# Kernel optimization log

Measured on AMD Instinct MI355X. Metric: run time of the kernel, lower is better.

The kernel has to match this reference:

```python
import jax, jax.numpy as jnp
import numpy as np
import math

NUM_EMBED = 1024
EMBED_FEATS = 256
IN_FEATS = 512
COMMITMENT_COST = 0.25
B, T = 16, 4096


def setup_inputs() -> dict:
    key = jax.random.key(0)
    k1, k2, k3, k4 = jax.random.split(key, 4)
    inputs = jax.random.normal(k1, (B, IN_FEATS, T), dtype=jnp.float32)
    # Conv1d(kernel_size=1) == per-position linear: weight [E, C_in], bias [E]
    proj_w = jax.random.normal(k2, (EMBED_FEATS, IN_FEATS), dtype=jnp.float32) / np.sqrt(IN_FEATS)
    proj_b = jax.random.normal(k3, (EMBED_FEATS,), dtype=jnp.float32) * 0.01
    embed = jax.random.normal(k4, (NUM_EMBED, EMBED_FEATS), dtype=jnp.float32)
    return {"inputs": inputs, "proj_w": proj_w, "proj_b": proj_b, "embed": embed}


def reference(inputs, proj_w, proj_b, embed):
    sg = jax.lax.stop_gradient
    b, c_in, t = inputs.shape
    # 1x1 conv projection then transpose(1,-1): [B, T, E]
    x = jnp.einsum('bct,ec->bte', inputs, proj_w) + proj_b
    flat = x.reshape(-1, EMBED_FEATS)  # [B*T, E]
    d2 = (jnp.sum(flat * flat, axis=1, keepdims=True)
          + jnp.sum(embed * embed, axis=1)
          - 2.0 * flat @ embed.T)  # [B*T, num_embed]
    q_idx = jnp.argmin(d2, axis=1)  # [B*T]
    # one-hot @ embed == direct gather (same math, same gradient structure)
    z_q = embed[q_idx].reshape(x.shape)  # [B, T, E]
    vq_loss = jnp.mean((z_q - sg(x)) ** 2)
    commitment_loss = jnp.mean((sg(z_q) - x) ** 2)
    loss = vq_loss + COMMITMENT_COST * commitment_loss
    z_q_st = x + sg(z_q - x)  # straight-through
    n_tokens = flat.shape[0]
    probs = jnp.zeros((NUM_EMBED,), dtype=jnp.float32).at[q_idx].add(1.0) / n_tokens
    log_perplexity = -jnp.sum(probs * jnp.log(probs + 1e-10))
    num_spatial = n_tokens / b
    kldiv_r = math.log(NUM_EMBED) * num_spatial * jnp.ones((b, 1), dtype=jnp.float32)
    z_q_out = jnp.swapaxes(z_q_st, 1, 2)  # [B, E, T]
    return z_q_out, loss, kldiv_r, log_perplexity
```

## Files before the change

kernel.cpp:

```cpp
#include <hip/hip_runtime.h>
#include <hip/hip_bf16.h>
#include <math.h>

#define TT   4096
#define BB   16
#define NTOK 65536
#define CIN  512
#define EF   256
#define NE   1024

typedef __attribute__((ext_vector_type(8))) short bf16x8;
typedef __attribute__((ext_vector_type(4))) float f32x4;

static __device__ __forceinline__ unsigned short f2bf(float f) {
  unsigned int u = __float_as_uint(f);
  u += 0x7fffu + ((u >> 16) & 1u);
  return (unsigned short)(u >> 16);
}

#define GLL(gsrc, ldst) \
  __builtin_amdgcn_global_load_lds((const __attribute__((address_space(1))) void*)(gsrc), \
                                   (__attribute__((address_space(3))) void*)(ldst), 16, 0, 0)

__global__ __launch_bounds__(256) void k_prep(const float* __restrict__ Wf,
                                              const float* __restrict__ Ef,
                                              unsigned short* __restrict__ Wbf,
                                              unsigned short* __restrict__ Ebf,
                                              float* __restrict__ e_norm) {
  int bid = blockIdx.x;
  if (bid < 512) {
    int i = bid * 256 + threadIdx.x;
    Wbf[i] = f2bf(Wf[i]);
  } else if (bid < 1536) {
    int i = (bid - 512) * 256 + threadIdx.x;
    Ebf[i] = f2bf(-2.0f * Ef[i]);
  } else {
    int w = threadIdx.x >> 6, l = threadIdx.x & 63;
    int k = (bid - 1536) * 4 + w;
    const float4 v4 = ((const float4*)(Ef + (size_t)k * EF))[l];
    float s = v4.x * v4.x + v4.y * v4.y + v4.z * v4.z + v4.w * v4.w;
    for (int off = 32; off; off >>= 1) s += __shfl_down(s, off);
    if (l == 0) e_norm[k] = s;
  }
}

__global__ __launch_bounds__(256, 2) void k_fused(const float* __restrict__ in,
                                                  const unsigned short* __restrict__ Wbf,
                                                  const float* __restrict__ bias,
                                                  const unsigned short* __restrict__ Ebf,
                                                  const float* __restrict__ e_norm,
                                                  int* __restrict__ bi_out,
                                                  unsigned int* __restrict__ hist,
                                                  float* __restrict__ sse) {
  __shared__ unsigned short lds[24576];
  unsigned short* as_ = lds;
  unsigned short* bs = lds + 4096;
  unsigned short* xs = lds;
  unsigned short* es = lds + 16384;

  int tid = threadIdx.x;
  int w = tid >> 6, l = tid & 63;
  int l15 = l & 15, quad = l >> 4;
  int tok0 = blockIdx.x * 64;
  int bidx = tok0 >> 12;
  int tg0 = tok0 & 4095;
  const float* src = in + (size_t)bidx * CIN * TT + tg0;

  f32x4 acc[4][4];
#pragma unroll
  for (int a = 0; a < 4; ++a)
#pragma unroll
    for (int b = 0; b < 4; ++b) acc[a][b] = (f32x4){0.f, 0.f, 0.f, 0.f};

  for (int ks = 0; ks < 8; ++ks) {
    int k0 = ks * 64;
#pragma unroll
    for (int i = 0; i < 8; ++i) {
      int g = i * 256 + tid;
      int row = g >> 3, pc = g & 7, lc = pc ^ (row & 7);
      GLL(Wbf + (size_t)row * CIN + k0 + lc * 8, bs + g * 8);
    }
#pragma unroll
    for (int cc = 0; cc < 2; ++cc) {
      float v[8];
      const float* s0 = src + (size_t)(k0 + w * 16 + cc * 8) * TT + l;
#pragma unroll
      for (int i = 0; i < 8; ++i) v[i] = s0[(size_t)i * TT];
      alignas(16) unsigned short tmp[8];
#pragma unroll
      for (int j = 0; j < 8; ++j) tmp[j] = f2bf(v[j]);
      int c8 = w * 2 + cc;
      int pc = c8 ^ (l & 7);
      *(bf16x8*)(as_ + l * 64 + pc * 8) = *(const bf16x8*)tmp;
    }
    __syncthreads();
#pragma unroll
    for (int s = 0; s < 2; ++s) {
      int lcb = s * 4 + quad;
      bf16x8 af[4], bfr[4];
#pragma unroll
      for (int msub = 0; msub < 4; ++msub) {
        int row = msub * 16 + l15;
        int pc = lcb ^ (row & 7);
        af[msub] = *(const bf16x8*)(as_ + row * 64 + pc * 8);
      }
#pragma unroll
      for (int nsub = 0; nsub < 4; ++nsub) {
        int row = w * 64 + nsub * 16 + l15;
        int pc = lcb ^ (row & 7);
        bfr[nsub] = *(const bf16x8*)(bs + row * 64 + pc * 8);
      }
#pragma unroll
      for (int msub = 0; msub < 4; ++msub)
#pragma unroll
        for (int nsub = 0; nsub < 4; ++nsub)
          acc[msub][nsub] = __builtin_amdgcn_mfma_f32_16x16x32_bf16(af[msub], bfr[nsub],
                                                                    acc[msub][nsub], 0, 0, 0);
    }
    __syncthreads();
  }

  float xsq = 0.f;
#pragma unroll
  for (int nsub = 0; nsub < 4; ++nsub) {
    float bv = bias[w * 64 + nsub * 16 + l15];
    int e = w * 64 + nsub * 16 + l15;
    int cx = e >> 3;
#pragma unroll
    for (int msub = 0; msub < 4; ++msub)
#pragma unroll
      for (int reg = 0; reg < 4; ++reg) {
        int m = msub * 16 + quad * 4 + reg;
        float x = acc[msub][nsub][reg] + bv;
        xsq += x * x;
        int pcx = cx ^ (m & 31);
        xs[m * 256 + pcx * 8 + (e & 7)] = f2bf(x);
      }
  }
  __syncthreads();

  float best_v[4][4];
  int best_i[4][4];
#pragma unroll
  for (int a = 0; a < 4; ++a)
#pragma unroll
    for (int b = 0; b < 4; ++b) { best_v[a][b] = 3.0e38f; best_i[a][b] = 0; }

  for (int chunk = 0; chunk < 8; ++chunk) {
    int c0 = chunk * 128;
    f32x4 dacc[4][2];
#pragma unroll
    for (int nsub = 0; nsub < 2; ++nsub) {
      float en = e_norm[c0 + w * 32 + nsub * 16 + l15];
#pragma unroll
      for (int msub = 0; msub < 4; ++msub) dacc[msub][nsub] = (f32x4){en, en, en, en};
    }
    for (int ks = 0; ks < 4; ++ks) {
      int k0 = ks * 64;
#pragma unroll
      for (int i = 0; i < 4; ++i) {
        int g = i * 256 + tid;
        int row = g >> 3, pc = g & 7, lc = pc ^ (row & 7);
        GLL(Ebf + (size_t)(c0 + row) * EF + k0 + lc * 8, es + g * 8);
      }
      __syncthreads();
#pragma unroll
      for (int s = 0; s < 2; ++s) {
        bf16x8 af[4], bfr[2];
        int cx = ks * 8 + s * 4 + quad;
#pragma unroll
        for (int msub = 0; msub < 4; ++msub) {
          int row = msub * 16 + l15;
          int pcx = cx ^ (row & 31);
          af[msub] = *(const bf16x8*)(xs + row * 256 + pcx * 8);
        }
        int ck = s * 4 + quad;
#pragma unroll
        for (int nsub = 0; nsub < 2; ++nsub) {
          int row = w * 32 + nsub * 16 + l15;
          int pc = ck ^ (row & 7);
          bfr[nsub] = *(const bf16x8*)(es + row * 64 + pc * 8);
        }
#pragma unroll
        for (int msub = 0; msub < 4; ++msub)
#pragma unroll
          for (int nsub = 0; nsub < 2; ++nsub)
            dacc[msub][nsub] = __builtin_amdgcn_mfma_f32_16x16x32_bf16(af[msub], bfr[nsub],
                                                                       dacc[msub][nsub], 0, 0, 0);
      }
      __syncthreads();
    }
#pragma unroll
    for (int msub = 0; msub < 4; ++msub)
#pragma unroll
      for (int nsub = 0; nsub < 2; ++nsub) {
        int code = c0 + w * 32 + nsub * 16 + l15;
#pragma unroll
        for (int reg = 0; reg < 4; ++reg) {
          float v = dacc[msub][nsub][reg];
          if (v < best_v[msub][reg]) { best_v[msub][reg] = v; best_i[msub][reg] = code; }
        }
      }
  }

#pragma unroll
  for (int msub = 0; msub < 4; ++msub)
#pragma unroll
    for (int reg = 0; reg < 4; ++reg) {
      float v = best_v[msub][reg];
      int idx = best_i[msub][reg];
#pragma unroll
      for (int off = 8; off; off >>= 1) {
        float ov = __shfl_xor(v, off, 16);
        int oi = __shfl_xor(idx, off, 16);
        if (ov < v || (ov == v && oi < idx)) { v = ov; idx = oi; }
      }
      best_v[msub][reg] = v;
      best_i[msub][reg] = idx;
    }
  float* red_v = (float*)es;
  int* red_i = (int*)(es) + 256;
  float* xred = (float*)(es) + 512;
  if (l15 == 0) {
#pragma unroll
    for (int msub = 0; msub < 4; ++msub)
#pragma unroll
      for (int reg = 0; reg < 4; ++reg) {
        int m = msub * 16 + quad * 4 + reg;
        red_v[w * 64 + m] = best_v[msub][reg];
        red_i[w * 64 + m] = best_i[msub][reg];
      }
  }
  for (int off = 32; off; off >>= 1) xsq += __shfl_down(xsq, off);
  if (l == 0) xred[w] = xsq;
  __syncthreads();
  if (tid < 64) {
    float v = red_v[tid];
    int idx = red_i[tid];
#pragma unroll
    for (int wj = 1; wj < 4; ++wj) {
      float ov = red_v[wj * 64 + tid];
      int oi = red_i[wj * 64 + tid];
      if (ov < v || (ov == v && oi < idx)) { v = ov; idx = oi; }
    }
    bi_out[tok0 + tid] = idx;
    atomicAdd(&hist[idx], 1u);
    float sv = v;
    for (int off = 32; off; off >>= 1) sv += __shfl_down(sv, off);
    if (tid == 0) atomicAdd(sse, sv + xred[0] + xred[1] + xred[2] + xred[3]);
  }
}

__global__ __launch_bounds__(256) void k_gather(const float* __restrict__ embed,
                                                const int* __restrict__ bi,
                                                float* __restrict__ out) {
  __shared__ float zq[128 * 65];
  __shared__ int idxs[128];
  int tid = threadIdx.x;
  int tok0 = blockIdx.x * 128;
  int e0 = blockIdx.y * 64;
  if (tid < 128) idxs[tid] = bi[tok0 + tid];
  __syncthreads();
  int l15 = tid & 15, tg = tid >> 4;
  for (int r = 0; r < 8; ++r) {
    int tl = r * 16 + tg;
    const float4 v = *(const float4*)(embed + (size_t)idxs[tl] * EF + e0 + l15 * 4);
    float* zr = zq + tl * 65 + l15 * 4;
    zr[0] = v.x; zr[1] = v.y; zr[2] = v.z; zr[3] = v.w;
  }
  __syncthreads();
  int b = tok0 >> 12, t0 = tok0 & 4095;
  int tl4 = (tid & 31) * 4;
  for (int r = 0; r < 8; ++r) {
    int e = r * 8 + (tid >> 5);
    float4 v;
    v.x = zq[(tl4 + 0) * 65 + e];
    v.y = zq[(tl4 + 1) * 65 + e];
    v.z = zq[(tl4 + 2) * 65 + e];
    v.w = zq[(tl4 + 3) * 65 + e];
    *(float4*)(out + ((size_t)(b * EF + e0 + e) << 12) + t0 + tl4) = v;
  }
}

__global__ __launch_bounds__(256) void k_final(const unsigned int* __restrict__ hist,
                                               const float* __restrict__ sse,
                                               float* __restrict__ out) {
  __shared__ float red[4];
  int tid = threadIdx.x;
  float local = 0.f;
  for (int i = tid; i < NE; i += 256) {
    float p = (float)hist[i] * (1.0f / 65536.0f);
    local -= p * logf(p + 1e-10f);
  }
  for (int off = 32; off; off >>= 1) local += __shfl_down(local, off);
  if ((tid & 63) == 0) red[tid >> 6] = local;
  __syncthreads();
  if (tid == 0) {
    float lp = red[0] + red[1] + red[2] + red[3];
    out[16777216] = 1.25f * sse[0] / 16777216.0f;
    out[16777233] = lp;
  }
  if (tid < 16) out[16777217 + tid] = 6.93147180559945f * 4096.0f;
}

extern "C" void kernel_launch(void* const* d_in, const int* in_sizes, int n_in,
                              void* d_out, int out_size, void* d_ws, size_t ws_size,
                              hipStream_t stream) {
  const float* inputs = (const float*)d_in[0];
  const float* proj_w = (const float*)d_in[1];
  const float* proj_b = (const float*)d_in[2];
  const float* embed = (const float*)d_in[3];
  float* out = (float*)d_out;
  char* ws = (char*)d_ws;

  unsigned short* Wbf  = (unsigned short*)(ws);
  unsigned short* Ebf  = (unsigned short*)(ws + 262144);
  float* e_norm        = (float*)(ws + 786432);
  int* bi              = (int*)(ws + 790528);
  unsigned int* hist   = (unsigned int*)(ws + 1052672);
  float* sse           = (float*)(ws + 1056768);
  if (ws_size < 1056772) return;

  hipMemsetAsync(ws + 1052672, 0, 4100, stream);

  k_prep<<<1792, 256, 0, stream>>>(proj_w, embed, Wbf, Ebf, e_norm);
  k_fused<<<1024, 256, 0, stream>>>(inputs, Wbf, proj_b, Ebf, e_norm, bi, hist, sse);
  k_gather<<<dim3(512, 4), 256, 0, stream>>>(embed, bi, out);
  k_final<<<1, 256, 0, stream>>>(hist, sse, out);
}
```

Baseline: 333.2 us.

## Restructure fused VQ kernel: 512 threads, register-prefetched inputs, double-buffered codebook

The fused projection+argmin kernel now processes 128 tokens per 512-thread block, doubling token-tile reuse of W and codebook loads. Input activations for the next K-step are prefetched into registers before the MFMA work, and the x tile is held in registers (full K=256) for the distance phase. Codebook chunks of 64 codes with full K are double-buffered in LDS so the next chunk's global-to-LDS load overlaps the current MFMAs, removing the inner K loop and half the barriers. This raises register pressure (launch bounds 512,4 may force spills) and LDS use to 64KB per block, which could limit occupancy.

```diff
diff --git a/kernel.cpp b/kernel.cpp
--- a/kernel.cpp
+++ b/kernel.cpp
@@ -44,7 +44,7 @@
   }
 }
 
-__global__ __launch_bounds__(256, 2) void k_fused(const float* __restrict__ in,
+__global__ __launch_bounds__(512, 4) void k_fused(const float* __restrict__ in,
                                                   const unsigned short* __restrict__ Wbf,
                                                   const float* __restrict__ bias,
                                                   const unsigned short* __restrict__ Ebf,
@@ -52,19 +52,18 @@
                                                   int* __restrict__ bi_out,
                                                   unsigned int* __restrict__ hist,
                                                   float* __restrict__ sse) {
-  __shared__ unsigned short lds[24576];
+  __shared__ unsigned short lds[32768];
   unsigned short* as_ = lds;
-  unsigned short* bs = lds + 4096;
-  unsigned short* xs = lds;
-  unsigned short* es = lds + 16384;
+  unsigned short* bs  = lds + 8192;
+  unsigned short* xs  = lds;
 
   int tid = threadIdx.x;
   int w = tid >> 6, l = tid & 63;
   int l15 = l & 15, quad = l >> 4;
-  int tok0 = blockIdx.x * 64;
-  int bidx = tok0 >> 12;
-  int tg0 = tok0 & 4095;
-  const float* src = in + (size_t)bidx * CIN * TT + tg0;
+  int tq = w & 1, eq = w >> 1;
+  int cg = w & 3, th = w >> 2;
+  int tok0 = blockIdx.x * 128;
+  const float* src = in + (size_t)(tok0 >> 12) * CIN * TT + (tok0 & 4095);
 
   f32x4 acc[4][4];
 #pragma unroll
@@ -72,43 +71,51 @@
 #pragma unroll
     for (int b = 0; b < 4; ++b) acc[a][b] = (f32x4){0.f, 0.f, 0.f, 0.f};
 
+  float v[16];
+  {
+    const float* s0 = src + (size_t)(cg * 16) * TT + th * 64 + l;
+#pragma unroll
+    for (int i = 0; i < 16; ++i) v[i] = s0[(size_t)i * TT];
+  }
   for (int ks = 0; ks < 8; ++ks) {
     int k0 = ks * 64;
 #pragma unroll
-    for (int i = 0; i < 8; ++i) {
-      int g = i * 256 + tid;
+    for (int i = 0; i < 4; ++i) {
+      int g = i * 512 + tid;
       int row = g >> 3, pc = g & 7, lc = pc ^ (row & 7);
       GLL(Wbf + (size_t)row * CIN + k0 + lc * 8, bs + g * 8);
     }
+    int trow = th * 64 + l;
 #pragma unroll
     for (int cc = 0; cc < 2; ++cc) {
-      float v[8];
-      const float* s0 = src + (size_t)(k0 + w * 16 + cc * 8) * TT + l;
-#pragma unroll
-      for (int i = 0; i < 8; ++i) v[i] = s0[(size_t)i * TT];
       alignas(16) unsigned short tmp[8];
 #pragma unroll
-      for (int j = 0; j < 8; ++j) tmp[j] = f2bf(v[j]);
-      int c8 = w * 2 + cc;
-      int pc = c8 ^ (l & 7);
-      *(bf16x8*)(as_ + l * 64 + pc * 8) = *(const bf16x8*)tmp;
+      for (int j = 0; j < 8; ++j) tmp[j] = f2bf(v[cc * 8 + j]);
+      int c8 = cg * 2 + cc;
+      int pc = c8 ^ (trow & 7);
+      *(bf16x8*)(as_ + trow * 64 + pc * 8) = *(const bf16x8*)tmp;
     }
     __syncthreads();
-#pragma unroll
-    for (int s = 0; s < 2; ++s) {
-      int lcb = s * 4 + quad;
+    if (ks < 7) {
+      const float* s0 = src + (size_t)(k0 + 64 + cg * 16) * TT + th * 64 + l;
+#pragma unroll
+      for (int i = 0; i < 16; ++i) v[i] = s0[(size_t)i * TT];
+    }
+#pragma unroll
+    for (int kstep = 0; kstep < 2; ++kstep) {
+      int ck = kstep * 4 + quad;
       bf16x8 af[4], bfr[4];
 #pragma unroll
       for (int msub = 0; msub < 4; ++msub) {
-        int row = msub * 16 + l15;
-        int pc = lcb ^ (row & 7);
-        af[msub] = *(const bf16x8*)(as_ + row * 64 + pc * 8);
+        int row = tq * 64 + msub * 16 + l15;
+        int pa = ck ^ (row & 7);
+        af[msub] = *(const bf16x8*)(as_ + row * 64 + pa * 8);
       }
 #pragma unroll
       for (int nsub = 0; nsub < 4; ++nsub) {
-        int row = w * 64 + nsub * 16 + l15;
-        int pc = lcb ^ (row & 7);
-        bfr[nsub] = *(const bf16x8*)(bs + row * 64 + pc * 8);
+        int row = eq * 64 + nsub * 16 + l15;
+        int pb = ck ^ (row & 7);
+        bfr[nsub] = *(const bf16x8*)(bs + row * 64 + pb * 8);
       }
 #pragma unroll
       for (int msub = 0; msub < 4; ++msub)
@@ -123,14 +130,14 @@
   float xsq = 0.f;
 #pragma unroll
   for (int nsub = 0; nsub < 4; ++nsub) {
-    float bv = bias[w * 64 + nsub * 16 + l15];
-    int e = w * 64 + nsub * 16 + l15;
+    int e = eq * 64 + nsub * 16 + l15;
+    float bv = bias[e];
     int cx = e >> 3;
 #pragma unroll
     for (int msub = 0; msub < 4; ++msub)
 #pragma unroll
       for (int reg = 0; reg < 4; ++reg) {
-        int m = msub * 16 + quad * 4 + reg;
+        int m = tq * 64 + msub * 16 + quad * 4 + reg;
         float x = acc[msub][nsub][reg] + bv;
         xsq += x * x;
         int pcx = cx ^ (m & 31);
@@ -139,115 +146,137 @@
   }
   __syncthreads();
 
-  float best_v[4][4];
-  int best_i[4][4];
-#pragma unroll
-  for (int a = 0; a < 4; ++a)
+  int g3 = w & 3, h = w >> 2;
+  bf16x8 af[2][8];
+#pragma unroll
+  for (int msub = 0; msub < 2; ++msub)
+#pragma unroll
+    for (int kst = 0; kst < 8; ++kst) {
+      int row = g3 * 32 + msub * 16 + l15;
+      int c32 = kst * 4 + quad;
+      int pcx = c32 ^ (row & 31);
+      af[msub][kst] = *(const bf16x8*)(xs + row * 256 + pcx * 8);
+    }
+  __syncthreads();
+
+#pragma unroll
+  for (int i = 0; i < 4; ++i) {
+    int g = i * 512 + tid;
+    int row = g >> 5, pcc = g & 31, lc = pcc ^ (row & 31);
+    GLL(Ebf + (size_t)row * EF + lc * 8, lds + g * 8);
+  }
+  float enn[2];
+  enn[0] = e_norm[h * 32 + l15];
+  enn[1] = e_norm[h * 32 + 16 + l15];
+  __syncthreads();
+
+  float best_v[2][4];
+  int best_i[2][4];
+#pragma unroll
+  for (int a = 0; a < 2; ++a)
 #pragma unroll
     for (int b = 0; b < 4; ++b) { best_v[a][b] = 3.0e38f; best_i[a][b] = 0; }
 
-  for (int chunk = 0; chunk < 8; ++chunk) {
-    int c0 = chunk * 128;
-    f32x4 dacc[4][2];
+  for (int chunk = 0; chunk < 16; ++chunk) {
+    int p = chunk & 1;
+    int c0 = chunk * 64;
+    unsigned short* eb = lds + p * 16384;
+    if (chunk < 15) {
+      unsigned short* ebn = lds + (p ^ 1) * 16384;
+#pragma unroll
+      for (int i = 0; i < 4; ++i) {
+        int g = i * 512 + tid;
+        int row = g >> 5, pcc = g & 31, lc = pcc ^ (row & 31);
+        GLL(Ebf + (size_t)(c0 + 64 + row) * EF + lc * 8, ebn + g * 8);
+      }
+    }
+    f32x4 dacc[2][2];
 #pragma unroll
     for (int nsub = 0; nsub < 2; ++nsub) {
-      float en = e_norm[c0 + w * 32 + nsub * 16 + l15];
-#pragma unroll
-      for (int msub = 0; msub < 4; ++msub) dacc[msub][nsub] = (f32x4){en, en, en, en};
-    }
-    for (int ks = 0; ks < 4; ++ks) {
-      int k0 = ks * 64;
-#pragma unroll
-      for (int i = 0; i < 4; ++i) {
-        int g = i * 256 + tid;
-        int row = g >> 3, pc = g & 7, lc = pc ^ (row & 7);
-        GLL(Ebf + (size_t)(c0 + row) * EF + k0 + lc * 8, es + g * 8);
-      }
-      __syncthreads();
-#pragma unroll
-      for (int s = 0; s < 2; ++s) {
-        bf16x8 af[4], bfr[2];
-        int cx = ks * 8 + s * 4 + quad;
-#pragma unroll
-        for (int msub = 0; msub < 4; ++msub) {
-          int row = msub * 16 + l15;
-          int pcx = cx ^ (row & 31);
-          af[msub] = *(const bf16x8*)(xs + row * 256 + pcx * 8);
+      float en = enn[nsub];
+#pragma unroll
+      for (int msub = 0; msub < 2; ++msub) dacc[msub][nsub] = (f32x4){en, en, en, en};
+    }
+    if (chunk < 15) {
+      enn[0] = e_norm[c0 + 64 + h * 32 + l15];
+      enn[1] = e_norm[c0 + 64 + h * 32 + 16 + l15];
+    }
+#pragma unroll
+    for (int nsub = 0; nsub < 2; ++nsub) {
+      int r = h * 32 + nsub * 16 + l15;
+#pragma unroll
+      for (int kst = 0; kst < 8; ++kst) {
+        int cc = kst * 4 + quad;
+        int pc = cc ^ (r & 31);
+        bf16x8 bfr = *(const bf16x8*)(eb + r * 256 + pc * 8);
+        dacc[0][nsub] = __builtin_amdgcn_mfma_f32_16x16x32_bf16(af[0][kst], bfr,
+                                                                dacc[0][nsub], 0, 0, 0);
+        dacc[1][nsub] = __builtin_amdgcn_mfma_f32_16x16x32_bf16(af[1][kst], bfr,
+                                                                dacc[1][nsub], 0, 0, 0);
+      }
+    }
+#pragma unroll
+    for (int msub = 0; msub < 2; ++msub)
+#pragma unroll
+      for (int nsub = 0; nsub < 2; ++nsub) {
+        int code = c0 + h * 32 + nsub * 16 + l15;
+#pragma unroll
+        for (int reg = 0; reg < 4; ++reg) {
+          float vv = dacc[msub][nsub][reg];
+          if (vv < best_v[msub][reg]) { best_v[msub][reg] = vv; best_i[msub][reg] = code; }
         }
-        int ck = s * 4 + quad;
-#pragma unroll
-        for (int nsub = 0; nsub < 2; ++nsub) {
-          int row = w * 32 + nsub * 16 + l15;
-          int pc = ck ^ (row & 7);
-          bfr[nsub] = *(const bf16x8*)(es + row * 64 + pc * 8);
-        }
-#pragma unroll
-        for (int msub = 0; msub < 4; ++msub)
-#pragma unroll
-          for (int nsub = 0; nsub < 2; ++nsub)
-            dacc[msub][nsub] = __builtin_amdgcn_mfma_f32_16x16x32_bf16(af[msub], bfr[nsub],
-                                                                       dacc[msub][nsub], 0, 0, 0);
-      }
-      __syncthreads();
-    }
-#pragma unroll
-    for (int msub = 0; msub < 4; ++msub)
-#pragma unroll
-      for (int nsub = 0; nsub < 2; ++nsub) {
-        int code = c0 + w * 32 + nsub * 16 + l15;
-#pragma unroll
-        for (int reg = 0; reg < 4; ++reg) {
-          float v = dacc[msub][nsub][reg];
-          if (v < best_v[msub][reg]) { best_v[msub][reg] = v; best_i[msub][reg] = code; }
-        }
-      }
-  }
-
-#pragma unroll
-  for (int msub = 0; msub < 4; ++msub)
+      }
+    __syncthreads();
+  }
+
+#pragma unroll
+  for (int msub = 0; msub < 2; ++msub)
 #pragma unroll
     for (int reg = 0; reg < 4; ++reg) {
-      float v = best_v[msub][reg];
+      float vv = best_v[msub][reg];
       int idx = best_i[msub][reg];
 #pragma unroll
       for (int off = 8; off; off >>= 1) {
-        float ov = __shfl_xor(v, off, 16);
+        float ov = __shfl_xor(vv, off, 16);
         int oi = __shfl_xor(idx, off, 16);
-        if (ov < v || (ov == v && oi < idx)) { v = ov; idx = oi; }
-      }
-      best_v[msub][reg] = v;
+        if (ov < vv || (ov == vv && oi < idx)) { vv = ov; idx = oi; }
+      }
+      best_v[msub][reg] = vv;
       best_i[msub][reg] = idx;
     }
-  float* red_v = (float*)es;
-  int* red_i = (int*)(es) + 256;
-  float* xred = (float*)(es) + 512;
+  float* red_v = (float*)lds;
+  int* red_i = (int*)lds + 256;
+  float* xred = (float*)lds + 512;
+  float* svred = (float*)lds + 520;
   if (l15 == 0) {
 #pragma unroll
-    for (int msub = 0; msub < 4; ++msub)
+    for (int msub = 0; msub < 2; ++msub)
 #pragma unroll
       for (int reg = 0; reg < 4; ++reg) {
-        int m = msub * 16 + quad * 4 + reg;
-        red_v[w * 64 + m] = best_v[msub][reg];
-        red_i[w * 64 + m] = best_i[msub][reg];
+        int tokloc = g3 * 32 + msub * 16 + quad * 4 + reg;
+        red_v[h * 128 + tokloc] = best_v[msub][reg];
+        red_i[h * 128 + tokloc] = best_i[msub][reg];
       }
   }
   for (int off = 32; off; off >>= 1) xsq += __shfl_down(xsq, off);
   if (l == 0) xred[w] = xsq;
   __syncthreads();
-  if (tid < 64) {
-    float v = red_v[tid];
-    int idx = red_i[tid];
-#pragma unroll
-    for (int wj = 1; wj < 4; ++wj) {
-      float ov = red_v[wj * 64 + tid];
-      int oi = red_i[wj * 64 + tid];
-      if (ov < v || (ov == v && oi < idx)) { v = ov; idx = oi; }
-    }
+  if (tid < 128) {
+    float v0 = red_v[tid], v1 = red_v[128 + tid];
+    int i0 = red_i[tid], i1 = red_i[128 + tid];
+    float vv; int idx;
+    if (v1 < v0 || (v1 == v0 && i1 < i0)) { vv = v1; idx = i1; } else { vv = v0; idx = i0; }
     bi_out[tok0 + tid] = idx;
     atomicAdd(&hist[idx], 1u);
-    float sv = v;
-    for (int off = 32; off; off >>= 1) sv += __shfl_down(sv, off);
-    if (tid == 0) atomicAdd(sse, sv + xred[0] + xred[1] + xred[2] + xred[3]);
+    for (int off = 32; off; off >>= 1) vv += __shfl_down(vv, off);
+    if ((tid & 63) == 0) svred[tid >> 6] = vv;
+  }
+  __syncthreads();
+  if (tid == 0) {
+    float tot = svred[0] + svred[1];
+#pragma unroll
+    for (int i = 0; i < 8; ++i) tot += xred[i];
+    atomicAdd(sse, tot);
   }
 }
 
@@ -324,7 +353,7 @@
   hipMemsetAsync(ws + 1052672, 0, 4100, stream);
 
   k_prep<<<1792, 256, 0, stream>>>(proj_w, embed, Wbf, Ebf, e_norm);
-  k_fused<<<1024, 256, 0, stream>>>(inputs, Wbf, proj_b, Ebf, e_norm, bi, hist, sse);
+  k_fused<<<512, 512, 0, stream>>>(inputs, Wbf, proj_b, Ebf, e_norm, bi, hist, sse);
   k_gather<<<dim3(512, 4), 256, 0, stream>>>(embed, bi, out);
   k_final<<<1, 256, 0, stream>>>(hist, sse, out);
 }
```

After: 327.3 us. No clear change (-1.8%).
